# Kernel optimization log

Measured on AMD Instinct MI355X. Metric: run time of the kernel, lower is better.

The kernel has to match this reference:

```python
import jax, jax.numpy as jnp
import numpy as np

N_NODES = 10000
IN_CH = 128
HID = 256
OUT_CH = 1
N_EDGES_ADJ = 320000  # avg degree 32
N_TARGET = 8192


def setup_inputs() -> dict:
    key = jax.random.key(0)
    ks = jax.random.split(key, 16)
    s = 0.05  # weight scale for numerical stability
    inp = {
        'x': jax.random.normal(ks[0], (N_NODES, IN_CH), jnp.float32),
        'adj_row': jax.random.randint(ks[1], (N_EDGES_ADJ,), 0, N_NODES),
        'adj_col': jax.random.randint(ks[2], (N_EDGES_ADJ,), 0, N_NODES),
        'tar_ei': jax.random.randint(ks[3], (2, N_TARGET), 0, N_NODES),
        'beta': jnp.ones((1,), jnp.float32),
        'W1': s * jax.random.normal(ks[4], (IN_CH, HID), jnp.float32),
        'b1': jnp.zeros((HID,), jnp.float32),
        'W2': s * jax.random.normal(ks[5], (HID, HID), jnp.float32),
        'b2': jnp.zeros((HID,), jnp.float32),
        'W3': s * jax.random.normal(ks[6], (HID, HID), jnp.float32),
        'b3': jnp.zeros((HID,), jnp.float32),
        'Wij1': s * jax.random.normal(ks[7], (IN_CH, HID), jnp.float32),
        'bij1': jnp.zeros((HID,), jnp.float32),
        'Wij2': s * jax.random.normal(ks[8], (HID, HID), jnp.float32),
        'bij2': jnp.zeros((HID,), jnp.float32),
        'Wl1': s * jax.random.normal(ks[9], (HID, HID), jnp.float32),
        'bl1': jnp.zeros((HID,), jnp.float32),
        'Wl2': s * jax.random.normal(ks[10], (HID, OUT_CH), jnp.float32),
        'bl2': jnp.zeros((OUT_CH,), jnp.float32),
    }
    return inp


def reference(x, adj_row, adj_col, tar_ei, beta, W1, b1, W2, b2, W3, b3,
              Wij1, bij1, Wij2, bij2, Wl1, bl1, Wl2, bl2):
    n = x.shape[0]
    # Binary adjacency (duplicates collapse to 1, matching SparseTensor semantics)
    A = jnp.zeros((n, n), x.dtype).at[adj_row, adj_col].set(1.0)
    xi = x[tar_ei[0]]  # [E, F]
    xj = x[tar_ei[1]]  # [E, F]
    # adjoverlap: common-neighbor indicator per target edge, then spmm_add with x
    cn_mask = A[tar_ei[0]] * A[tar_ei[1]]          # [E, N]
    cn_x = cn_mask @ x                              # [E, F] sum of features over common neighbors
    # xcnlin: Linear-ReLU-Linear-ReLU-Linear (eval mode: dropout=identity, ln=identity)
    xcn = jax.nn.relu(cn_x @ W1 + b1)
    xcn = jax.nn.relu(xcn @ W2 + b2)
    xcn = xcn @ W3 + b3
    # xijlin: Linear-ReLU-Linear
    xij = jax.nn.relu((xi * xj) @ Wij1 + bij1) @ Wij2 + bij2
    # lin head: Linear-ReLU-Linear
    h = jax.nn.relu((xcn * beta + xij) @ Wl1 + bl1)
    return h @ Wl2 + bl2  # [E, 1]
```

## Files before the change

kernel.cpp:

```cpp
#include <hip/hip_runtime.h>
#include <hip/hip_bf16.h>

#define N_NODES 10000
#define IN_CH 128
#define HID 256
#define E_TAR 8192
#define N_EDGES 320000
#define CSR_MAX 128
#define BM 32

typedef short bf16x8 __attribute__((ext_vector_type(8)));
typedef short bf16x4 __attribute__((ext_vector_type(4)));
typedef float f32x4 __attribute__((ext_vector_type(4)));

__device__ __forceinline__ unsigned short f2bf(float f) {
  union { float f; unsigned u; } v; v.f = f;
  unsigned r = v.u + 0x7fffu + ((v.u >> 16) & 1u);
  return (unsigned short)(r >> 16);
}
__device__ __forceinline__ float bf2f(unsigned short h) {
  union { unsigned u; float f; } v; v.u = ((unsigned)h) << 16; return v.f;
}

__global__ void prep_w(const float* __restrict__ W1, const float* __restrict__ W2,
                       const float* __restrict__ W3, const float* __restrict__ Wij1,
                       const float* __restrict__ Wij2, const float* __restrict__ Wl1,
                       unsigned short* __restrict__ wts, uint4* __restrict__ degz) {
  if (blockIdx.x >= 320) {
    int i = (blockIdx.x - 320) * 256 + threadIdx.x;
    if (i < (N_NODES + 3) / 4) degz[i] = (uint4){0u, 0u, 0u, 0u};
    return;
  }
  int bid = blockIdx.x;
  const float* W; unsigned short* O; int K, t;
  if      (bid <  32) { W = W1;   O = wts;          K = 128; t = bid; }
  else if (bid <  96) { W = W2;   O = wts + 32768;  K = 256; t = bid - 32; }
  else if (bid < 160) { W = W3;   O = wts + 98304;  K = 256; t = bid - 96; }
  else if (bid < 192) { W = Wij1; O = wts + 163840; K = 128; t = bid - 160; }
  else if (bid < 256) { W = Wij2; O = wts + 196608; K = 256; t = bid - 192; }
  else                { W = Wl1;  O = wts + 262144; K = 256; t = bid - 256; }
  int tpk = K / 32, tk = t % tpk, tn = t / tpk;
  __shared__ float tile[32][33];
  int tid = threadIdx.x;
  int c = tid & 31, r0 = tid >> 5;
  #pragma unroll
  for (int rr = 0; rr < 32; rr += 8)
    tile[r0 + rr][c] = W[(size_t)(tk * 32 + r0 + rr) * 256 + tn * 32 + c];
  __syncthreads();
  #pragma unroll
  for (int rr = 0; rr < 32; rr += 8)
    O[(size_t)(tn * 32 + r0 + rr) * K + tk * 32 + c] = f2bf(tile[c][r0 + rr]);
}

__global__ void scatter_csr(const int* __restrict__ row, const int* __restrict__ col,
                            int* __restrict__ deg, int* __restrict__ csr) {
  int k = blockIdx.x * 256 + threadIdx.x;
  if (k < N_EDGES) {
    int r = row[k], c = col[k];
    int p = atomicAdd(&deg[r], 1);
    if (p < CSR_MAX) csr[(size_t)r * CSR_MAX + p] = c;
  }
}

__global__ __launch_bounds__(512, 2) void fused_all(
    const int* __restrict__ deg, const int* __restrict__ csr,
    const int* __restrict__ tar, const float* __restrict__ x,
    const unsigned short* __restrict__ wts,
    const float* __restrict__ b1, const float* __restrict__ b2, const float* __restrict__ b3,
    const float* __restrict__ bij1, const float* __restrict__ bij2, const float* __restrict__ bl1,
    const float* __restrict__ Wl2, const float* __restrict__ bl2,
    const float* __restrict__ betaPtr, float* __restrict__ out)
{
  __shared__ unsigned short P[BM][264];
  __shared__ unsigned short Q[BM][264];

  int m0 = blockIdx.x * BM;
  int tid = threadIdx.x;
  int lane = tid & 63, wv = tid >> 6;
  int wn = wv * 32;
  int l15 = lane & 15, kg = (lane >> 4) * 8, rq = (lane >> 4) * 4;

  bf16x8 Bv0, Bv1, Bv2, Bv3, Bv4, Bv5, Bv6, Bv7;
  bf16x8 Bv8, Bv9, Bv10, Bv11, Bv12, Bv13, Bv14, Bv15;
  f32x4 a00, a01, a10, a11;
  f32x4 x00, x01, x10, x11;

#define LB128(WT) { \
    const unsigned short* _p = (WT) + (size_t)(wn + l15) * 128 + kg; \
    const unsigned short* _q = (WT) + (size_t)(wn + 16 + l15) * 128 + kg; \
    Bv0 = *(const bf16x8*)_p;        Bv1 = *(const bf16x8*)(_p + 32); \
    Bv2 = *(const bf16x8*)(_p + 64); Bv3 = *(const bf16x8*)(_p + 96); \
    Bv8 = *(const bf16x8*)_q;        Bv9 = *(const bf16x8*)(_q + 32); \
    Bv10 = *(const bf16x8*)(_q + 64); Bv11 = *(const bf16x8*)(_q + 96); }

#define LB256(WT) { \
    const unsigned short* _p = (WT) + (size_t)(wn + l15) * 256 + kg; \
    const unsigned short* _q = (WT) + (size_t)(wn + 16 + l15) * 256 + kg; \
    Bv0 = *(const bf16x8*)_p;         Bv1 = *(const bf16x8*)(_p + 32); \
    Bv2 = *(const bf16x8*)(_p + 64);  Bv3 = *(const bf16x8*)(_p + 96); \
    Bv4 = *(const bf16x8*)(_p + 128); Bv5 = *(const bf16x8*)(_p + 160); \
    Bv6 = *(const bf16x8*)(_p + 192); Bv7 = *(const bf16x8*)(_p + 224); \
    Bv8 = *(const bf16x8*)_q;         Bv9 = *(const bf16x8*)(_q + 32); \
    Bv10 = *(const bf16x8*)(_q + 64); Bv11 = *(const bf16x8*)(_q + 96); \
    Bv12 = *(const bf16x8*)(_q + 128); Bv13 = *(const bf16x8*)(_q + 160); \
    Bv14 = *(const bf16x8*)(_q + 192); Bv15 = *(const bf16x8*)(_q + 224); }

#define ST(S, S8, AA) { \
    bf16x8 _a0 = *(const bf16x8*)&AA[l15][S * 32 + kg]; \
    bf16x8 _a1 = *(const bf16x8*)&AA[16 + l15][S * 32 + kg]; \
    a00 = __builtin_amdgcn_mfma_f32_16x16x32_bf16(_a0, Bv##S,  a00, 0, 0, 0); \
    a10 = __builtin_amdgcn_mfma_f32_16x16x32_bf16(_a1, Bv##S,  a10, 0, 0, 0); \
    a01 = __builtin_amdgcn_mfma_f32_16x16x32_bf16(_a0, Bv##S8, a01, 0, 0, 0); \
    a11 = __builtin_amdgcn_mfma_f32_16x16x32_bf16(_a1, Bv##S8, a11, 0, 0, 0); }

#define CL128(AA) ST(0, 8, AA) ST(1, 9, AA) ST(2, 10, AA) ST(3, 11, AA)
#define CL256(AA) CL128(AA) ST(4, 12, AA) ST(5, 13, AA) ST(6, 14, AA) ST(7, 15, AA)

#define ZA { a00 = (f32x4){0,0,0,0}; a01 = (f32x4){0,0,0,0}; \
             a10 = (f32x4){0,0,0,0}; a11 = (f32x4){0,0,0,0}; }

#define EPIW(DST, BS0, BS1, RELU) { \
    _Pragma("unroll") for (int i = 0; i < 4; ++i) { \
      float v0 = a00[i] + BS0, v1 = a10[i] + BS0; \
      float v2 = a01[i] + BS1, v3 = a11[i] + BS1; \
      if (RELU) { v0 = fmaxf(v0, 0.f); v1 = fmaxf(v1, 0.f); \
                  v2 = fmaxf(v2, 0.f); v3 = fmaxf(v3, 0.f); } \
      DST[rq + i][wn + l15]           = f2bf(v0); \
      DST[16 + rq + i][wn + l15]      = f2bf(v1); \
      DST[rq + i][wn + 16 + l15]      = f2bf(v2); \
      DST[16 + rq + i][wn + 16 + l15] = f2bf(v3); } }

  LB128(wts);

  int row = tid >> 4, seg = tid & 15;
  int gi = tar[m0 + row], gj = tar[E_TAR + m0 + row];
  const float* xip = x + (size_t)gi * IN_CH + seg * 8;
  const float* xjp = x + (size_t)gj * IN_CH + seg * 8;
  f32x4 xi0 = *(const f32x4*)xip, xi1 = *(const f32x4*)(xip + 4);
  f32x4 xj0 = *(const f32x4*)xjp, xj1 = *(const f32x4*)(xjp + 4);
  float bv1_0   = b1[wn + l15],   bv1_1   = b1[wn + 16 + l15];
  float bv2_0   = b2[wn + l15],   bv2_1   = b2[wn + 16 + l15];
  float bv3_0   = b3[wn + l15],   bv3_1   = b3[wn + 16 + l15];
  float bvij1_0 = bij1[wn + l15], bvij1_1 = bij1[wn + 16 + l15];
  float bvij2_0 = bij2[wn + l15], bvij2_1 = bij2[wn + 16 + l15];
  float bvl1_0  = bl1[wn + l15],  bvl1_1  = bl1[wn + 16 + l15];
  float beta_v = betaPtr[0];
  f32x4 w2v = *(const f32x4*)&Wl2[lane * 4];

  float g0[4] = {0.f, 0.f, 0.f, 0.f}, g1[4] = {0.f, 0.f, 0.f, 0.f};
  #pragma unroll
  for (int q = 0; q < 4; ++q) {
    int e = m0 + wv * 4 + q;
    int ti_ = tar[e], tj_ = tar[E_TAR + e];
    int di_ = min(deg[ti_], CSR_MAX), dj_ = min(deg[tj_], CSR_MAX);
    int a_ = (di_ <= dj_) ? ti_ : tj_;
    int b_ = (di_ <= dj_) ? tj_ : ti_;
    int da_ = min(di_, dj_), db_ = max(di_, dj_);
    const int* la = csr + (size_t)a_ * CSR_MAX;
    const int* lb = csr + (size_t)b_ * CSR_MAX;
    for (int ab = 0; ab < da_; ab += 64) {
      int t = ab + lane;
      int at = (t < da_) ? la[t] : -1;
      bool hit = false;
      for (int bb = 0; bb < db_; bb += 64) {
        int u = bb + lane;
        int bl = (u < db_) ? lb[u] : -2;
        int lim = db_ - bb; if (lim > 64) lim = 64;
        for (int j = 0; j < lim; ++j) {
          int bj = __shfl(bl, j);
          hit |= (at == bj);
        }
      }
      bool dup = false;
      for (int pb = 0; pb <= ab; pb += 64) {
        int u = pb + lane;
        int av = (u < da_) ? la[u] : -3;
        int lim = da_ - pb; if (lim > 64) lim = 64;
        for (int k2 = 0; k2 < lim; ++k2) {
          int ak = __shfl(av, k2);
          dup |= ((pb + k2) < t && ak == at);
        }
      }
      bool good = (t < da_) && hit && !dup;
      unsigned long long bal = __ballot(good);
      while (bal) {
        int src = __ffsll(bal) - 1;
        bal &= bal - 1;
        int nb = __shfl(at, src);
        const float* xr = x + (size_t)nb * IN_CH;
        g0[q] += xr[lane];
        g1[q] += xr[lane + 64];
      }
    }
  }
  #pragma unroll
  for (int q = 0; q < 4; ++q) {
    int r = wv * 4 + q;
    P[r][lane]      = f2bf(g0[q]);
    P[r][64 + lane] = f2bf(g1[q]);
  }
  __syncthreads();

  ZA; CL128(P); LB256(wts + 32768); EPIW(Q, bv1_0, bv1_1, true);
  __syncthreads();

  ZA; CL256(Q); LB256(wts + 98304); EPIW(P, bv2_0, bv2_1, true);
  __syncthreads();

  ZA; CL256(P); LB128(wts + 163840);
  #pragma unroll
  for (int i = 0; i < 4; ++i) {
    x00[i] = a00[i] + bv3_0; x10[i] = a10[i] + bv3_0;
    x01[i] = a01[i] + bv3_1; x11[i] = a11[i] + bv3_1;
  }
  __syncthreads();

  {
    unsigned short tmp[8];
    #pragma unroll
    for (int u = 0; u < 4; ++u) {
      tmp[u]     = f2bf(xi0[u] * xj0[u]);
      tmp[4 + u] = f2bf(xi1[u] * xj1[u]);
    }
    *(bf16x8*)&P[row][seg * 8] = *(bf16x8*)tmp;
  }
  __syncthreads();

  ZA; CL128(P); LB256(wts + 196608); EPIW(Q, bvij1_0, bvij1_1, true);
  __syncthreads();

  ZA; CL256(Q); LB256(wts + 262144);
  #pragma unroll
  for (int i = 0; i < 4; ++i) {
    float v0 = a00[i] + bvij2_0 + beta_v * x00[i];
    float v1 = a10[i] + bvij2_0 + beta_v * x10[i];
    float v2 = a01[i] + bvij2_1 + beta_v * x01[i];
    float v3 = a11[i] + bvij2_1 + beta_v * x11[i];
    P[rq + i][wn + l15]           = f2bf(v0);
    P[16 + rq + i][wn + l15]      = f2bf(v1);
    P[rq + i][wn + 16 + l15]      = f2bf(v2);
    P[16 + rq + i][wn + 16 + l15] = f2bf(v3);
  }
  __syncthreads();

  ZA; CL256(P); EPIW(Q, bvl1_0, bvl1_1, true);
  __syncthreads();

  {
    float bl2v = bl2[0];
    #pragma unroll
    for (int rr = 0; rr < 4; ++rr) {
      int r = wv * 4 + rr;
      bf16x4 qv = *(const bf16x4*)&Q[r][lane * 4];
      float s = 0.f;
      #pragma unroll
      for (int u = 0; u < 4; ++u) s += bf2f((unsigned short)qv[u]) * w2v[u];
      #pragma unroll
      for (int off = 32; off; off >>= 1) s += __shfl_down(s, off);
      if (lane == 0) out[m0 + r] = s + bl2v;
    }
  }
}

extern "C" void kernel_launch(void* const* d_in, const int* in_sizes, int n_in,
                              void* d_out, int out_size, void* d_ws, size_t ws_size,
                              hipStream_t stream) {
  const float* x      = (const float*)d_in[0];
  const int*   adj_r  = (const int*)d_in[1];
  const int*   adj_c  = (const int*)d_in[2];
  const int*   tar    = (const int*)d_in[3];
  const float* beta   = (const float*)d_in[4];
  const float* W1     = (const float*)d_in[5];
  const float* b1     = (const float*)d_in[6];
  const float* W2     = (const float*)d_in[7];
  const float* b2     = (const float*)d_in[8];
  const float* W3     = (const float*)d_in[9];
  const float* b3     = (const float*)d_in[10];
  const float* Wij1   = (const float*)d_in[11];
  const float* bij1   = (const float*)d_in[12];
  const float* Wij2   = (const float*)d_in[13];
  const float* bij2   = (const float*)d_in[14];
  const float* Wl1    = (const float*)d_in[15];
  const float* bl1    = (const float*)d_in[16];
  const float* Wl2    = (const float*)d_in[17];
  const float* bl2    = (const float*)d_in[18];

  char* ws = (char*)d_ws;
  int*            deg = (int*)ws;
  int*            csr = (int*)(ws + (size_t)1 * 1024 * 1024);
  unsigned short* wts = (unsigned short*)(ws + (size_t)8 * 1024 * 1024);

  prep_w<<<330, 256, 0, stream>>>(W1, W2, W3, Wij1, Wij2, Wl1, wts, (uint4*)deg);
  scatter_csr<<<(N_EDGES + 255) / 256, 256, 0, stream>>>(adj_r, adj_c, deg, csr);
  fused_all<<<E_TAR / BM, 512, 0, stream>>>(deg, csr, tar, x, wts,
                                            b1, b2, b3, bij1, bij2, bl1,
                                            Wl2, bl2, beta, (float*)d_out);
}
```

Before: 75.26 us.

## Split common-neighbor gather into its own kernel and halve MLP row tile

The fused kernel is split in two. A standalone cn_gather kernel (256 threads, 4 edges per wave) computes the common-neighbor feature sums and writes them as bf16 to a workspace buffer. A separate mlp kernel then runs the MLP chain with 16-row tiles and launch bounds allowing 4 blocks per CU. The aim is to stop the irregular, divergent intersection loop from stalling the MFMA pipeline and to raise occupancy and block count for both phases. The cost is an extra launch plus a global round trip of the cn features, and with half as many rows per block each weight load is reused over fewer rows.

```diff
diff --git a/kernel.cpp b/kernel.cpp
--- a/kernel.cpp
+++ b/kernel.cpp
@@ -7,7 +7,7 @@
 #define E_TAR 8192
 #define N_EDGES 320000
 #define CSR_MAX 128
-#define BM 32
+#define BM 16
 
 typedef short bf16x8 __attribute__((ext_vector_type(8)));
 typedef short bf16x4 __attribute__((ext_vector_type(4)));
@@ -62,95 +62,14 @@
   }
 }
 
-__global__ __launch_bounds__(512, 2) void fused_all(
-    const int* __restrict__ deg, const int* __restrict__ csr,
-    const int* __restrict__ tar, const float* __restrict__ x,
-    const unsigned short* __restrict__ wts,
-    const float* __restrict__ b1, const float* __restrict__ b2, const float* __restrict__ b3,
-    const float* __restrict__ bij1, const float* __restrict__ bij2, const float* __restrict__ bl1,
-    const float* __restrict__ Wl2, const float* __restrict__ bl2,
-    const float* __restrict__ betaPtr, float* __restrict__ out)
-{
-  __shared__ unsigned short P[BM][264];
-  __shared__ unsigned short Q[BM][264];
-
-  int m0 = blockIdx.x * BM;
-  int tid = threadIdx.x;
-  int lane = tid & 63, wv = tid >> 6;
-  int wn = wv * 32;
-  int l15 = lane & 15, kg = (lane >> 4) * 8, rq = (lane >> 4) * 4;
-
-  bf16x8 Bv0, Bv1, Bv2, Bv3, Bv4, Bv5, Bv6, Bv7;
-  bf16x8 Bv8, Bv9, Bv10, Bv11, Bv12, Bv13, Bv14, Bv15;
-  f32x4 a00, a01, a10, a11;
-  f32x4 x00, x01, x10, x11;
-
-#define LB128(WT) { \
-    const unsigned short* _p = (WT) + (size_t)(wn + l15) * 128 + kg; \
-    const unsigned short* _q = (WT) + (size_t)(wn + 16 + l15) * 128 + kg; \
-    Bv0 = *(const bf16x8*)_p;        Bv1 = *(const bf16x8*)(_p + 32); \
-    Bv2 = *(const bf16x8*)(_p + 64); Bv3 = *(const bf16x8*)(_p + 96); \
-    Bv8 = *(const bf16x8*)_q;        Bv9 = *(const bf16x8*)(_q + 32); \
-    Bv10 = *(const bf16x8*)(_q + 64); Bv11 = *(const bf16x8*)(_q + 96); }
-
-#define LB256(WT) { \
-    const unsigned short* _p = (WT) + (size_t)(wn + l15) * 256 + kg; \
-    const unsigned short* _q = (WT) + (size_t)(wn + 16 + l15) * 256 + kg; \
-    Bv0 = *(const bf16x8*)_p;         Bv1 = *(const bf16x8*)(_p + 32); \
-    Bv2 = *(const bf16x8*)(_p + 64);  Bv3 = *(const bf16x8*)(_p + 96); \
-    Bv4 = *(const bf16x8*)(_p + 128); Bv5 = *(const bf16x8*)(_p + 160); \
-    Bv6 = *(const bf16x8*)(_p + 192); Bv7 = *(const bf16x8*)(_p + 224); \
-    Bv8 = *(const bf16x8*)_q;         Bv9 = *(const bf16x8*)(_q + 32); \
-    Bv10 = *(const bf16x8*)(_q + 64); Bv11 = *(const bf16x8*)(_q + 96); \
-    Bv12 = *(const bf16x8*)(_q + 128); Bv13 = *(const bf16x8*)(_q + 160); \
-    Bv14 = *(const bf16x8*)(_q + 192); Bv15 = *(const bf16x8*)(_q + 224); }
-
-#define ST(S, S8, AA) { \
-    bf16x8 _a0 = *(const bf16x8*)&AA[l15][S * 32 + kg]; \
-    bf16x8 _a1 = *(const bf16x8*)&AA[16 + l15][S * 32 + kg]; \
-    a00 = __builtin_amdgcn_mfma_f32_16x16x32_bf16(_a0, Bv##S,  a00, 0, 0, 0); \
-    a10 = __builtin_amdgcn_mfma_f32_16x16x32_bf16(_a1, Bv##S,  a10, 0, 0, 0); \
-    a01 = __builtin_amdgcn_mfma_f32_16x16x32_bf16(_a0, Bv##S8, a01, 0, 0, 0); \
-    a11 = __builtin_amdgcn_mfma_f32_16x16x32_bf16(_a1, Bv##S8, a11, 0, 0, 0); }
-
-#define CL128(AA) ST(0, 8, AA) ST(1, 9, AA) ST(2, 10, AA) ST(3, 11, AA)
-#define CL256(AA) CL128(AA) ST(4, 12, AA) ST(5, 13, AA) ST(6, 14, AA) ST(7, 15, AA)
-
-#define ZA { a00 = (f32x4){0,0,0,0}; a01 = (f32x4){0,0,0,0}; \
-             a10 = (f32x4){0,0,0,0}; a11 = (f32x4){0,0,0,0}; }
-
-#define EPIW(DST, BS0, BS1, RELU) { \
-    _Pragma("unroll") for (int i = 0; i < 4; ++i) { \
-      float v0 = a00[i] + BS0, v1 = a10[i] + BS0; \
-      float v2 = a01[i] + BS1, v3 = a11[i] + BS1; \
-      if (RELU) { v0 = fmaxf(v0, 0.f); v1 = fmaxf(v1, 0.f); \
-                  v2 = fmaxf(v2, 0.f); v3 = fmaxf(v3, 0.f); } \
-      DST[rq + i][wn + l15]           = f2bf(v0); \
-      DST[16 + rq + i][wn + l15]      = f2bf(v1); \
-      DST[rq + i][wn + 16 + l15]      = f2bf(v2); \
-      DST[16 + rq + i][wn + 16 + l15] = f2bf(v3); } }
-
-  LB128(wts);
-
-  int row = tid >> 4, seg = tid & 15;
-  int gi = tar[m0 + row], gj = tar[E_TAR + m0 + row];
-  const float* xip = x + (size_t)gi * IN_CH + seg * 8;
-  const float* xjp = x + (size_t)gj * IN_CH + seg * 8;
-  f32x4 xi0 = *(const f32x4*)xip, xi1 = *(const f32x4*)(xip + 4);
-  f32x4 xj0 = *(const f32x4*)xjp, xj1 = *(const f32x4*)(xjp + 4);
-  float bv1_0   = b1[wn + l15],   bv1_1   = b1[wn + 16 + l15];
-  float bv2_0   = b2[wn + l15],   bv2_1   = b2[wn + 16 + l15];
-  float bv3_0   = b3[wn + l15],   bv3_1   = b3[wn + 16 + l15];
-  float bvij1_0 = bij1[wn + l15], bvij1_1 = bij1[wn + 16 + l15];
-  float bvij2_0 = bij2[wn + l15], bvij2_1 = bij2[wn + 16 + l15];
-  float bvl1_0  = bl1[wn + l15],  bvl1_1  = bl1[wn + 16 + l15];
-  float beta_v = betaPtr[0];
-  f32x4 w2v = *(const f32x4*)&Wl2[lane * 4];
-
+__global__ void cn_gather(const int* __restrict__ deg, const int* __restrict__ csr,
+                          const int* __restrict__ tar, const float* __restrict__ x,
+                          unsigned short* __restrict__ cnx) {
+  int lane = threadIdx.x & 63, wv = threadIdx.x >> 6;
   float g0[4] = {0.f, 0.f, 0.f, 0.f}, g1[4] = {0.f, 0.f, 0.f, 0.f};
   #pragma unroll
   for (int q = 0; q < 4; ++q) {
-    int e = m0 + wv * 4 + q;
+    int e = blockIdx.x * 16 + wv * 4 + q;
     int ti_ = tar[e], tj_ = tar[E_TAR + e];
     int di_ = min(deg[ti_], CSR_MAX), dj_ = min(deg[tj_], CSR_MAX);
     int a_ = (di_ <= dj_) ? ti_ : tj_;
@@ -195,10 +114,87 @@
   }
   #pragma unroll
   for (int q = 0; q < 4; ++q) {
-    int r = wv * 4 + q;
-    P[r][lane]      = f2bf(g0[q]);
-    P[r][64 + lane] = f2bf(g1[q]);
-  }
+    int e = blockIdx.x * 16 + wv * 4 + q;
+    cnx[(size_t)e * IN_CH + lane]      = f2bf(g0[q]);
+    cnx[(size_t)e * IN_CH + 64 + lane] = f2bf(g1[q]);
+  }
+}
+
+__global__ __launch_bounds__(512, 4) void mlp(
+    const unsigned short* __restrict__ cnx, const int* __restrict__ tar,
+    const float* __restrict__ x, const unsigned short* __restrict__ wts,
+    const float* __restrict__ b1, const float* __restrict__ b2, const float* __restrict__ b3,
+    const float* __restrict__ bij1, const float* __restrict__ bij2, const float* __restrict__ bl1,
+    const float* __restrict__ Wl2, const float* __restrict__ bl2,
+    const float* __restrict__ betaPtr, float* __restrict__ out)
+{
+  __shared__ unsigned short P[BM][264];
+  __shared__ unsigned short Q[BM][264];
+
+  int m0 = blockIdx.x * BM;
+  int tid = threadIdx.x;
+  int lane = tid & 63, wv = tid >> 6;
+  int wn = wv * 32;
+  int l15 = lane & 15, kg = (lane >> 4) * 8, rq = (lane >> 4) * 4;
+
+  bf16x8 Bv0, Bv1, Bv2, Bv3, Bv4, Bv5, Bv6, Bv7;
+  bf16x8 Bv8, Bv9, Bv10, Bv11, Bv12, Bv13, Bv14, Bv15;
+  f32x4 a00, a01;
+  f32x4 x00, x01;
+
+#define LB128(WT) { \
+    const unsigned short* _p = (WT) + (size_t)(wn + l15) * 128 + kg; \
+    const unsigned short* _q = (WT) + (size_t)(wn + 16 + l15) * 128 + kg; \
+    Bv0 = *(const bf16x8*)_p;        Bv1 = *(const bf16x8*)(_p + 32); \
+    Bv2 = *(const bf16x8*)(_p + 64); Bv3 = *(const bf16x8*)(_p + 96); \
+    Bv8 = *(const bf16x8*)_q;        Bv9 = *(const bf16x8*)(_q + 32); \
+    Bv10 = *(const bf16x8*)(_q + 64); Bv11 = *(const bf16x8*)(_q + 96); }
+
+#define LB256(WT) { \
+    const unsigned short* _p = (WT) + (size_t)(wn + l15) * 256 + kg; \
+    const unsigned short* _q = (WT) + (size_t)(wn + 16 + l15) * 256 + kg; \
+    Bv0 = *(const bf16x8*)_p;         Bv1 = *(const bf16x8*)(_p + 32); \
+    Bv2 = *(const bf16x8*)(_p + 64);  Bv3 = *(const bf16x8*)(_p + 96); \
+    Bv4 = *(const bf16x8*)(_p + 128); Bv5 = *(const bf16x8*)(_p + 160); \
+    Bv6 = *(const bf16x8*)(_p + 192); Bv7 = *(const bf16x8*)(_p + 224); \
+    Bv8 = *(const bf16x8*)_q;         Bv9 = *(const bf16x8*)(_q + 32); \
+    Bv10 = *(const bf16x8*)(_q + 64); Bv11 = *(const bf16x8*)(_q + 96); \
+    Bv12 = *(const bf16x8*)(_q + 128); Bv13 = *(const bf16x8*)(_q + 160); \
+    Bv14 = *(const bf16x8*)(_q + 192); Bv15 = *(const bf16x8*)(_q + 224); }
+
+#define ST(S, S8, AA) { \
+    bf16x8 _a0 = *(const bf16x8*)&AA[l15][S * 32 + kg]; \
+    a00 = __builtin_amdgcn_mfma_f32_16x16x32_bf16(_a0, Bv##S,  a00, 0, 0, 0); \
+    a01 = __builtin_amdgcn_mfma_f32_16x16x32_bf16(_a0, Bv##S8, a01, 0, 0, 0); }
+
+#define CL128(AA) ST(0, 8, AA) ST(1, 9, AA) ST(2, 10, AA) ST(3, 11, AA)
+#define CL256(AA) CL128(AA) ST(4, 12, AA) ST(5, 13, AA) ST(6, 14, AA) ST(7, 15, AA)
+
+#define ZA { a00 = (f32x4){0,0,0,0}; a01 = (f32x4){0,0,0,0}; }
+
+#define EPIW(DST, BS0, BS1, RELU) { \
+    _Pragma("unroll") for (int i = 0; i < 4; ++i) { \
+      float v0 = a00[i] + BS0, v2 = a01[i] + BS1; \
+      if (RELU) { v0 = fmaxf(v0, 0.f); v2 = fmaxf(v2, 0.f); } \
+      DST[rq + i][wn + l15]      = f2bf(v0); \
+      DST[rq + i][wn + 16 + l15] = f2bf(v2); } }
+
+  LB128(wts);
+
+  int row = tid >> 5, s = tid & 31;
+  int gi = tar[m0 + row], gj = tar[E_TAR + m0 + row];
+  f32x4 xi = *(const f32x4*)(x + (size_t)gi * IN_CH + s * 4);
+  f32x4 xj = *(const f32x4*)(x + (size_t)gj * IN_CH + s * 4);
+  float bv1_0   = b1[wn + l15],   bv1_1   = b1[wn + 16 + l15];
+  float bv2_0   = b2[wn + l15],   bv2_1   = b2[wn + 16 + l15];
+  float bv3_0   = b3[wn + l15],   bv3_1   = b3[wn + 16 + l15];
+  float bvij1_0 = bij1[wn + l15], bvij1_1 = bij1[wn + 16 + l15];
+  float bvij2_0 = bij2[wn + l15], bvij2_1 = bij2[wn + 16 + l15];
+  float bvl1_0  = bl1[wn + l15],  bvl1_1  = bl1[wn + 16 + l15];
+  float beta_v = betaPtr[0];
+  f32x4 w2v = *(const f32x4*)&Wl2[lane * 4];
+
+  *(bf16x4*)&P[row][s * 4] = *(const bf16x4*)&cnx[(size_t)(m0 + row) * IN_CH + s * 4];
   __syncthreads();
 
   ZA; CL128(P); LB256(wts + 32768); EPIW(Q, bv1_0, bv1_1, true);
@@ -209,20 +205,14 @@
 
   ZA; CL256(P); LB128(wts + 163840);
   #pragma unroll
-  for (int i = 0; i < 4; ++i) {
-    x00[i] = a00[i] + bv3_0; x10[i] = a10[i] + bv3_0;
-    x01[i] = a01[i] + bv3_1; x11[i] = a11[i] + bv3_1;
-  }
+  for (int i = 0; i < 4; ++i) { x00[i] = a00[i] + bv3_0; x01[i] = a01[i] + bv3_1; }
   __syncthreads();
 
   {
-    unsigned short tmp[8];
+    unsigned short tmp[4];
     #pragma unroll
-    for (int u = 0; u < 4; ++u) {
-      tmp[u]     = f2bf(xi0[u] * xj0[u]);
-      tmp[4 + u] = f2bf(xi1[u] * xj1[u]);
-    }
-    *(bf16x8*)&P[row][seg * 8] = *(bf16x8*)tmp;
+    for (int u = 0; u < 4; ++u) tmp[u] = f2bf(xi[u] * xj[u]);
+    *(bf16x4*)&P[row][s * 4] = *(bf16x4*)tmp;
   }
   __syncthreads();
 
@@ -233,13 +223,9 @@
   #pragma unroll
   for (int i = 0; i < 4; ++i) {
     float v0 = a00[i] + bvij2_0 + beta_v * x00[i];
-    float v1 = a10[i] + bvij2_0 + beta_v * x10[i];
     float v2 = a01[i] + bvij2_1 + beta_v * x01[i];
-    float v3 = a11[i] + bvij2_1 + beta_v * x11[i];
-    P[rq + i][wn + l15]           = f2bf(v0);
-    P[16 + rq + i][wn + l15]      = f2bf(v1);
-    P[rq + i][wn + 16 + l15]      = f2bf(v2);
-    P[16 + rq + i][wn + 16 + l15] = f2bf(v3);
+    P[rq + i][wn + l15]      = f2bf(v0);
+    P[rq + i][wn + 16 + l15] = f2bf(v2);
   }
   __syncthreads();
 
@@ -249,15 +235,15 @@
   {
     float bl2v = bl2[0];
     #pragma unroll
-    for (int rr = 0; rr < 4; ++rr) {
-      int r = wv * 4 + rr;
+    for (int rr = 0; rr < 2; ++rr) {
+      int r = wv * 2 + rr;
       bf16x4 qv = *(const bf16x4*)&Q[r][lane * 4];
-      float s = 0.f;
+      float sacc = 0.f;
       #pragma unroll
-      for (int u = 0; u < 4; ++u) s += bf2f((unsigned short)qv[u]) * w2v[u];
+      for (int u = 0; u < 4; ++u) sacc += bf2f((unsigned short)qv[u]) * w2v[u];
       #pragma unroll
-      for (int off = 32; off; off >>= 1) s += __shfl_down(s, off);
-      if (lane == 0) out[m0 + r] = s + bl2v;
+      for (int off = 32; off; off >>= 1) sacc += __shfl_down(sacc, off);
+      if (lane == 0) out[m0 + r] = sacc + bl2v;
     }
   }
 }
@@ -289,10 +275,12 @@
   int*            deg = (int*)ws;
   int*            csr = (int*)(ws + (size_t)1 * 1024 * 1024);
   unsigned short* wts = (unsigned short*)(ws + (size_t)8 * 1024 * 1024);
+  unsigned short* cnx = (unsigned short*)(ws + (size_t)10 * 1024 * 1024);
 
   prep_w<<<330, 256, 0, stream>>>(W1, W2, W3, Wij1, Wij2, Wl1, wts, (uint4*)deg);
   scatter_csr<<<(N_EDGES + 255) / 256, 256, 0, stream>>>(adj_r, adj_c, deg, csr);
-  fused_all<<<E_TAR / BM, 512, 0, stream>>>(deg, csr, tar, x, wts,
-                                            b1, b2, b3, bij1, bij2, bl1,
-                                            Wl2, bl2, beta, (float*)d_out);
-}
+  cn_gather<<<E_TAR / 16, 256, 0, stream>>>(deg, csr, tar, x, cnx);
+  mlp<<<E_TAR / BM, 512, 0, stream>>>(cnx, tar, x, wts,
+                                      b1, b2, b3, bij1, bij2, bl1,
+                                      Wl2, bl2, beta, (float*)d_out);
+}
```

After: 95.04 us. +26.3%, slower.
